# Kernel tuning notes

Measured on AMD Instinct MI355X. Metric: run time of the kernel, lower is better.

Reference implementation:

```python
import jax, jax.numpy as jnp
import numpy as np
import math

PATCH_SIZE = 64      # patch size at level resolution
LEVEL_RES = 512      # level resolution
TARGET_SIZE = 16     # mask patch output size
EXTRACT_SIZE = 16    # target_patch_grid_size for features
TEMPERATURE = 1.5    # temperature for entropy confidence


def _grid_sample_border(img, grid):
    """Bilinear grid_sample, padding_mode='border', align_corners=False.
    img: [C, H, W]; grid: [..., 2] (x, y) in [-1, 1]. Returns [C, ...]."""
    C, H, W = img.shape
    x = jnp.clip(((grid[..., 0] + 1.0) * W - 1.0) * 0.5, 0.0, W - 1.0)
    y = jnp.clip(((grid[..., 1] + 1.0) * H - 1.0) * 0.5, 0.0, H - 1.0)
    x0 = jnp.floor(x)
    y0 = jnp.floor(y)
    x1 = jnp.minimum(x0 + 1.0, W - 1.0)
    y1 = jnp.minimum(y0 + 1.0, H - 1.0)
    wx = x - x0
    wy = y - y0
    x0i, x1i = x0.astype(jnp.int32), x1.astype(jnp.int32)
    y0i, y1i = y0.astype(jnp.int32), y1.astype(jnp.int32)
    flat = img.reshape(C, H * W)
    gather = lambda yi, xi: jnp.take(flat, yi * W + xi, axis=1)  # [C, ...]
    v00 = gather(y0i, x0i)
    v01 = gather(y0i, x1i)
    v10 = gather(y1i, x0i)
    v11 = gather(y1i, x1i)
    top = v00 * (1.0 - wx) + v01 * wx
    bot = v10 * (1.0 - wx) + v11 * wx
    return top * (1.0 - wy) + bot * wy


def _make_grid(fh, fw, half, res, tsize):
    """fh, fw: [B, K] patch centers in pixel units at resolution `res`.
    Returns sampling grid [B, K, tsize, tsize, 2] in (x, y) normalized coords."""
    cy = fh / res * 2.0 - 1.0
    cx = fw / res * 2.0 - 1.0
    off = jnp.linspace(-half, half, tsize, dtype=jnp.float32)
    gy, gx = jnp.meshgrid(off, off, indexing='ij')
    offs = jnp.stack([gx, gy], axis=-1)             # [t, t, 2]
    centers = jnp.stack([cx, cy], axis=-1)          # [B, K, 2]
    return centers[:, :, None, None, :] + offs[None, None]


def setup_inputs() -> dict:
    key = jax.random.key(0)
    k1, k2, k3, k4 = jax.random.split(key, 4)
    B, K, D, N = 4, 32, 512, 4096
    features = jax.random.normal(k1, (B, N, D), jnp.float32)
    mask = jax.random.normal(k2, (B, 1, LEVEL_RES, LEVEL_RES), jnp.float32)
    logits = jax.random.normal(k3, (B, K, 1, 64, 64), jnp.float32)
    coords = jax.random.randint(k4, (B, K, 2), 0, LEVEL_RES - PATCH_SIZE, jnp.int32)
    return {"features": features, "mask": mask, "logits": logits, "coords": coords}


def reference(features, mask, logits, coords):
    B, N, D = features.shape
    K = coords.shape[1]
    ags = int(round(N ** 0.5))  # actual feature grid size

    # --- entropy confidence ---
    p = jnp.clip(jax.nn.sigmoid(logits / TEMPERATURE), 1e-6, 1.0 - 1e-6)
    ent = -(p * jnp.log(p) + (1.0 - p) * jnp.log(1.0 - p))
    confidence = 1.0 - ent / math.log(2.0)
    if confidence.shape[2] > 1:
        confidence = confidence.mean(axis=2, keepdims=True)

    ch = coords[..., 0].astype(jnp.float32)
    cw = coords[..., 1].astype(jnp.float32)

    # --- mask patches (grid_sample over full-res mask) ---
    grid_m = _make_grid(ch + PATCH_SIZE / 2, cw + PATCH_SIZE / 2,
                        PATCH_SIZE / LEVEL_RES, LEVEL_RES, TARGET_SIZE)
    mp = jax.vmap(_grid_sample_border)(mask, grid_m)          # [B, 1, K, t, t]
    mask_patches = jnp.transpose(mp, (0, 2, 1, 3, 4))         # [B, K, 1, t, t]

    # --- patch features (grid_sample over token feature grid) ---
    scale = ags / LEVEL_RES
    psf = max(1, int(PATCH_SIZE * scale))                     # patch size in feature px
    grid_f = _make_grid(ch * scale + psf / 2, cw * scale + psf / 2,
                        psf / ags, ags, EXTRACT_SIZE)
    feats_sp = jnp.transpose(features.reshape(B, ags, ags, D), (0, 3, 1, 2))
    pf = jax.vmap(_grid_sample_border)(feats_sp, grid_f)      # [B, D, K, E, E]
    patch_features = jnp.transpose(pf, (0, 2, 3, 4, 1)).reshape(
        B, K, EXTRACT_SIZE * EXTRACT_SIZE, D)                 # [B, K, E*E, D]

    return confidence, mask_patches, patch_features
```

## Files before the change

### kernel.cpp

```cpp
#include <hip/hip_runtime.h>
#include <math.h>

#define Bn   4
#define Kn   32
#define Dn   512
#define Nn   4096
#define AGS  64
#define RES  512
#define TS   16
#define OFF0   (-0.125f)
#define OFFSTEP (0.25f / 15.0f)

__device__ __forceinline__ float unnorm_clip(float g, float size) {
    float v = ((g + 1.0f) * size - 1.0f) * 0.5f;
    return fminf(fmaxf(v, 0.0f), size - 1.0f);
}

__global__ void conf_kernel(const float* __restrict__ logits,
                            float* __restrict__ out, int n) {
    int i = blockIdx.x * blockDim.x + threadIdx.x;
    if (i >= n) return;
    float x = logits[i] * (1.0f / 1.5f);
    float p = 1.0f / (1.0f + expf(-x));
    p = fminf(fmaxf(p, 1e-6f), 1.0f - 1e-6f);
    float ent = -(p * logf(p) + (1.0f - p) * logf(1.0f - p));
    out[i] = 1.0f - ent * 1.4426950408889634f;
}

__global__ void mask_kernel(const float* __restrict__ mask,
                            const int* __restrict__ coords,
                            float* __restrict__ out) {
    int idx = blockIdx.x * blockDim.x + threadIdx.x;
    if (idx >= Bn * Kn * TS * TS) return;
    int j  = idx & 15;
    int i  = (idx >> 4) & 15;
    int bk = idx >> 8;
    int b  = bk >> 5;

    float ch = (float)coords[bk * 2 + 0];
    float cw = (float)coords[bk * 2 + 1];
    float cy = (ch + 32.0f) * (2.0f / 512.0f) - 1.0f;
    float cx = (cw + 32.0f) * (2.0f / 512.0f) - 1.0f;
    float gx = cx + (OFF0 + j * OFFSTEP);
    float gy = cy + (OFF0 + i * OFFSTEP);

    float x = unnorm_clip(gx, 512.0f);
    float y = unnorm_clip(gy, 512.0f);
    float x0f = floorf(x), y0f = floorf(y);
    int x0 = (int)x0f, y0 = (int)y0f;
    int x1 = min(x0 + 1, 511), y1 = min(y0 + 1, 511);
    float wx = x - x0f, wy = y - y0f;

    const float* mb = mask + (size_t)b * RES * RES;
    float v00 = mb[y0 * RES + x0];
    float v01 = mb[y0 * RES + x1];
    float v10 = mb[y1 * RES + x0];
    float v11 = mb[y1 * RES + x1];
    float top = v00 * (1.0f - wx) + v01 * wx;
    float bot = v10 * (1.0f - wx) + v11 * wx;
    out[idx] = top * (1.0f - wy) + bot * wy;
}

__global__ void feat_kernel(const float* __restrict__ features,
                            const int* __restrict__ coords,
                            float* __restrict__ out) {
    int tid = blockIdx.x * blockDim.x + threadIdx.x;
    int dc     = tid & 127;
    int sample = tid >> 7;
    if (sample >= Bn * Kn * TS * TS) return;
    int j  = sample & 15;
    int i  = (sample >> 4) & 15;
    int bk = sample >> 8;
    int b  = bk >> 5;

    float ch = (float)coords[bk * 2 + 0];
    float cw = (float)coords[bk * 2 + 1];
    float cy = (ch * 0.125f + 4.0f) * (2.0f / 64.0f) - 1.0f;
    float cx = (cw * 0.125f + 4.0f) * (2.0f / 64.0f) - 1.0f;
    float gx = cx + (OFF0 + j * OFFSTEP);
    float gy = cy + (OFF0 + i * OFFSTEP);

    float x = unnorm_clip(gx, 64.0f);
    float y = unnorm_clip(gy, 64.0f);
    float x0f = floorf(x), y0f = floorf(y);
    int x0 = (int)x0f, y0 = (int)y0f;
    int x1 = min(x0 + 1, 63), y1 = min(y0 + 1, 63);
    float wx = x - x0f, wy = y - y0f;

    const float4* f = (const float4*)(features + (size_t)b * Nn * Dn);
    float4 v00 = f[(y0 * AGS + x0) * 128 + dc];
    float4 v01 = f[(y0 * AGS + x1) * 128 + dc];
    float4 v10 = f[(y1 * AGS + x0) * 128 + dc];
    float4 v11 = f[(y1 * AGS + x1) * 128 + dc];

    float4 top, bot, r;
    top.x = v00.x * (1.0f - wx) + v01.x * wx;
    top.y = v00.y * (1.0f - wx) + v01.y * wx;
    top.z = v00.z * (1.0f - wx) + v01.z * wx;
    top.w = v00.w * (1.0f - wx) + v01.w * wx;
    bot.x = v10.x * (1.0f - wx) + v11.x * wx;
    bot.y = v10.y * (1.0f - wx) + v11.y * wx;
    bot.z = v10.z * (1.0f - wx) + v11.z * wx;
    bot.w = v10.w * (1.0f - wx) + v11.w * wx;
    r.x = top.x * (1.0f - wy) + bot.x * wy;
    r.y = top.y * (1.0f - wy) + bot.y * wy;
    r.z = top.z * (1.0f - wy) + bot.z * wy;
    r.w = top.w * (1.0f - wy) + bot.w * wy;

    ((float4*)out)[(size_t)sample * 128 + dc] = r;
}

extern "C" void kernel_launch(void* const* d_in, const int* in_sizes, int n_in,
                              void* d_out, int out_size, void* d_ws, size_t ws_size,
                              hipStream_t stream) {
    const float* features = (const float*)d_in[0];
    const float* mask     = (const float*)d_in[1];
    const float* logits   = (const float*)d_in[2];
    const int*   coords   = (const int*)d_in[3];

    float* out_conf = (float*)d_out;
    float* out_mask = out_conf + (size_t)Bn * Kn * 64 * 64;
    float* out_feat = out_mask + (size_t)Bn * Kn * TS * TS;

    int n_conf = Bn * Kn * 64 * 64;
    conf_kernel<<<(n_conf + 255) / 256, 256, 0, stream>>>(logits, out_conf, n_conf);

    int n_mask = Bn * Kn * TS * TS;
    mask_kernel<<<(n_mask + 255) / 256, 256, 0, stream>>>(mask, coords, out_mask);

    int n_feat_threads = Bn * Kn * TS * TS * 128;
    feat_kernel<<<(n_feat_threads + 255) / 256, 256, 0, stream>>>(features, coords, out_feat);
}
```

Baseline: 114.4 us.

## Fuse three sampling kernels into one launch with nontemporal stores

Merges the confidence, mask-sampling and feature-sampling kernels into a single launch that partitions the thread index range across the three tasks. Each feature thread now handles two float4 chunks, and the confidence path is vectorized four-wide with fast exp/log and an algebraically simplified entropy. All outputs use nontemporal stores. The goal is to remove launch gaps and cut per-thread index overhead on the write-bound feature output. The risk is that dropping the probability clamp and using fast intrinsics changes numerics slightly, and the mixed branches can cause divergence at the region boundaries.

```diff
diff --git a/kernel.cpp b/kernel.cpp
--- a/kernel.cpp
+++ b/kernel.cpp
@@ -8,106 +8,129 @@
 #define AGS  64
 #define RES  512
 #define TS   16
-#define OFF0   (-0.125f)
+#define OFF0    (-0.125f)
 #define OFFSTEP (0.25f / 15.0f)
+
+typedef float f32x4 __attribute__((ext_vector_type(4)));
+
+#define FEAT_T (Bn * Kn * TS * TS * 64)
+#define CONF_T (Bn * Kn * 64 * 64 / 4)
+#define MASK_T (Bn * Kn * TS * TS)
+#define TOTAL_T (FEAT_T + CONF_T + MASK_T)
 
 __device__ __forceinline__ float unnorm_clip(float g, float size) {
     float v = ((g + 1.0f) * size - 1.0f) * 0.5f;
     return fminf(fmaxf(v, 0.0f), size - 1.0f);
 }
 
-__global__ void conf_kernel(const float* __restrict__ logits,
-                            float* __restrict__ out, int n) {
-    int i = blockIdx.x * blockDim.x + threadIdx.x;
-    if (i >= n) return;
-    float x = logits[i] * (1.0f / 1.5f);
-    float p = 1.0f / (1.0f + expf(-x));
-    p = fminf(fmaxf(p, 1e-6f), 1.0f - 1e-6f);
-    float ent = -(p * logf(p) + (1.0f - p) * logf(1.0f - p));
-    out[i] = 1.0f - ent * 1.4426950408889634f;
+__device__ __forceinline__ float conf_elem(float logit) {
+    float s = logit * (1.0f / 1.5f);
+    float e = __expf(-s);
+    float p = 1.0f / (1.0f + e);
+    float ent = __logf(1.0f + e) + (1.0f - p) * s;
+    return 1.0f - ent * 1.4426950408889634f;
 }
 
-__global__ void mask_kernel(const float* __restrict__ mask,
-                            const int* __restrict__ coords,
-                            float* __restrict__ out) {
-    int idx = blockIdx.x * blockDim.x + threadIdx.x;
-    if (idx >= Bn * Kn * TS * TS) return;
-    int j  = idx & 15;
-    int i  = (idx >> 4) & 15;
-    int bk = idx >> 8;
-    int b  = bk >> 5;
+__global__ __launch_bounds__(256) void fused_kernel(
+    const float* __restrict__ features,
+    const float* __restrict__ mask,
+    const float* __restrict__ logits,
+    const int*   __restrict__ coords,
+    float* __restrict__ out_conf,
+    float* __restrict__ out_mask,
+    float* __restrict__ out_feat) {
 
-    float ch = (float)coords[bk * 2 + 0];
-    float cw = (float)coords[bk * 2 + 1];
-    float cy = (ch + 32.0f) * (2.0f / 512.0f) - 1.0f;
-    float cx = (cw + 32.0f) * (2.0f / 512.0f) - 1.0f;
-    float gx = cx + (OFF0 + j * OFFSTEP);
-    float gy = cy + (OFF0 + i * OFFSTEP);
+    int tid = blockIdx.x * blockDim.x + threadIdx.x;
 
-    float x = unnorm_clip(gx, 512.0f);
-    float y = unnorm_clip(gy, 512.0f);
-    float x0f = floorf(x), y0f = floorf(y);
-    int x0 = (int)x0f, y0 = (int)y0f;
-    int x1 = min(x0 + 1, 511), y1 = min(y0 + 1, 511);
-    float wx = x - x0f, wy = y - y0f;
+    if (tid < FEAT_T) {
+        int dc     = tid & 63;
+        int sample = tid >> 6;
+        int j  = sample & 15;
+        int i  = (sample >> 4) & 15;
+        int bk = sample >> 8;
+        int b  = bk >> 5;
 
-    const float* mb = mask + (size_t)b * RES * RES;
-    float v00 = mb[y0 * RES + x0];
-    float v01 = mb[y0 * RES + x1];
-    float v10 = mb[y1 * RES + x0];
-    float v11 = mb[y1 * RES + x1];
-    float top = v00 * (1.0f - wx) + v01 * wx;
-    float bot = v10 * (1.0f - wx) + v11 * wx;
-    out[idx] = top * (1.0f - wy) + bot * wy;
-}
+        float ch = (float)coords[bk * 2 + 0];
+        float cw = (float)coords[bk * 2 + 1];
+        float cy = (ch * 0.125f + 4.0f) * (2.0f / 64.0f) - 1.0f;
+        float cx = (cw * 0.125f + 4.0f) * (2.0f / 64.0f) - 1.0f;
+        float gx = cx + (OFF0 + j * OFFSTEP);
+        float gy = cy + (OFF0 + i * OFFSTEP);
 
-__global__ void feat_kernel(const float* __restrict__ features,
-                            const int* __restrict__ coords,
-                            float* __restrict__ out) {
-    int tid = blockIdx.x * blockDim.x + threadIdx.x;
-    int dc     = tid & 127;
-    int sample = tid >> 7;
-    if (sample >= Bn * Kn * TS * TS) return;
-    int j  = sample & 15;
-    int i  = (sample >> 4) & 15;
-    int bk = sample >> 8;
-    int b  = bk >> 5;
+        float x = unnorm_clip(gx, 64.0f);
+        float y = unnorm_clip(gy, 64.0f);
+        float x0f = floorf(x), y0f = floorf(y);
+        int x0 = (int)x0f, y0 = (int)y0f;
+        int x1 = min(x0 + 1, 63), y1 = min(y0 + 1, 63);
+        float wx = x - x0f, wy = y - y0f;
 
-    float ch = (float)coords[bk * 2 + 0];
-    float cw = (float)coords[bk * 2 + 1];
-    float cy = (ch * 0.125f + 4.0f) * (2.0f / 64.0f) - 1.0f;
-    float cx = (cw * 0.125f + 4.0f) * (2.0f / 64.0f) - 1.0f;
-    float gx = cx + (OFF0 + j * OFFSTEP);
-    float gy = cy + (OFF0 + i * OFFSTEP);
+        const f32x4* f = (const f32x4*)(features + (size_t)b * Nn * Dn);
+        int r00 = (y0 * AGS + x0) * 128 + dc;
+        int r01 = (y0 * AGS + x1) * 128 + dc;
+        int r10 = (y1 * AGS + x0) * 128 + dc;
+        int r11 = (y1 * AGS + x1) * 128 + dc;
 
-    float x = unnorm_clip(gx, 64.0f);
-    float y = unnorm_clip(gy, 64.0f);
-    float x0f = floorf(x), y0f = floorf(y);
-    int x0 = (int)x0f, y0 = (int)y0f;
-    int x1 = min(x0 + 1, 63), y1 = min(y0 + 1, 63);
-    float wx = x - x0f, wy = y - y0f;
+        f32x4 a00 = f[r00],      a01 = f[r01],      a10 = f[r10],      a11 = f[r11];
+        f32x4 b00 = f[r00 + 64], b01 = f[r01 + 64], b10 = f[r10 + 64], b11 = f[r11 + 64];
 
-    const float4* f = (const float4*)(features + (size_t)b * Nn * Dn);
-    float4 v00 = f[(y0 * AGS + x0) * 128 + dc];
-    float4 v01 = f[(y0 * AGS + x1) * 128 + dc];
-    float4 v10 = f[(y1 * AGS + x0) * 128 + dc];
-    float4 v11 = f[(y1 * AGS + x1) * 128 + dc];
+        float w00 = (1.0f - wx) * (1.0f - wy);
+        float w01 = wx * (1.0f - wy);
+        float w10 = (1.0f - wx) * wy;
+        float w11 = wx * wy;
 
-    float4 top, bot, r;
-    top.x = v00.x * (1.0f - wx) + v01.x * wx;
-    top.y = v00.y * (1.0f - wx) + v01.y * wx;
-    top.z = v00.z * (1.0f - wx) + v01.z * wx;
-    top.w = v00.w * (1.0f - wx) + v01.w * wx;
-    bot.x = v10.x * (1.0f - wx) + v11.x * wx;
-    bot.y = v10.y * (1.0f - wx) + v11.y * wx;
-    bot.z = v10.z * (1.0f - wx) + v11.z * wx;
-    bot.w = v10.w * (1.0f - wx) + v11.w * wx;
-    r.x = top.x * (1.0f - wy) + bot.x * wy;
-    r.y = top.y * (1.0f - wy) + bot.y * wy;
-    r.z = top.z * (1.0f - wy) + bot.z * wy;
-    r.w = top.w * (1.0f - wy) + bot.w * wy;
+        f32x4 ra = a00 * w00 + a01 * w01 + a10 * w10 + a11 * w11;
+        f32x4 rb = b00 * w00 + b01 * w01 + b10 * w10 + b11 * w11;
 
-    ((float4*)out)[(size_t)sample * 128 + dc] = r;
+        f32x4* op = (f32x4*)out_feat + (size_t)sample * 128 + dc;
+        __builtin_nontemporal_store(ra, op);
+        __builtin_nontemporal_store(rb, op + 64);
+        return;
+    }
+    tid -= FEAT_T;
+
+    if (tid < CONF_T) {
+        f32x4 v = ((const f32x4*)logits)[tid];
+        f32x4 r;
+        r.x = conf_elem(v.x);
+        r.y = conf_elem(v.y);
+        r.z = conf_elem(v.z);
+        r.w = conf_elem(v.w);
+        __builtin_nontemporal_store(r, (f32x4*)out_conf + tid);
+        return;
+    }
+    tid -= CONF_T;
+
+    {
+        int idx = tid;
+        int j  = idx & 15;
+        int i  = (idx >> 4) & 15;
+        int bk = idx >> 8;
+        int b  = bk >> 5;
+
+        float ch = (float)coords[bk * 2 + 0];
+        float cw = (float)coords[bk * 2 + 1];
+        float cy = (ch + 32.0f) * (2.0f / 512.0f) - 1.0f;
+        float cx = (cw + 32.0f) * (2.0f / 512.0f) - 1.0f;
+        float gx = cx + (OFF0 + j * OFFSTEP);
+        float gy = cy + (OFF0 + i * OFFSTEP);
+
+        float x = unnorm_clip(gx, 512.0f);
+        float y = unnorm_clip(gy, 512.0f);
+        float x0f = floorf(x), y0f = floorf(y);
+        int x0 = (int)x0f, y0 = (int)y0f;
+        int x1 = min(x0 + 1, 511), y1 = min(y0 + 1, 511);
+        float wx = x - x0f, wy = y - y0f;
+
+        const float* mb = mask + (size_t)b * RES * RES;
+        float v00 = mb[y0 * RES + x0];
+        float v01 = mb[y0 * RES + x1];
+        float v10 = mb[y1 * RES + x0];
+        float v11 = mb[y1 * RES + x1];
+        float top = v00 * (1.0f - wx) + v01 * wx;
+        float bot = v10 * (1.0f - wx) + v11 * wx;
+        float r = top * (1.0f - wy) + bot * wy;
+        __builtin_nontemporal_store(r, out_mask + idx);
+    }
 }
 
 extern "C" void kernel_launch(void* const* d_in, const int* in_sizes, int n_in,
@@ -122,12 +145,6 @@
     float* out_mask = out_conf + (size_t)Bn * Kn * 64 * 64;
     float* out_feat = out_mask + (size_t)Bn * Kn * TS * TS;
 
-    int n_conf = Bn * Kn * 64 * 64;
-    conf_kernel<<<(n_conf + 255) / 256, 256, 0, stream>>>(logits, out_conf, n_conf);
-
-    int n_mask = Bn * Kn * TS * TS;
-    mask_kernel<<<(n_mask + 255) / 256, 256, 0, stream>>>(mask, coords, out_mask);
-
-    int n_feat_threads = Bn * Kn * TS * TS * 128;
-    feat_kernel<<<(n_feat_threads + 255) / 256, 256, 0, stream>>>(features, coords, out_feat);
+    fused_kernel<<<TOTAL_T / 256, 256, 0, stream>>>(
+        features, mask, logits, coords, out_conf, out_mask, out_feat);
 }
```

Result: no change. 113.2 us (-1.0%).
